# Performance work log

Measured on AMD Instinct MI355X. Metric: run time of the kernel, lower is better.

Reference implementation:

```python
import jax, jax.numpy as jnp
import numpy as np

NEG_SLOPE = 0.2
NUM_NODES = 100000
NUM_EDGES = 200000
NNZ = 1600000
IN_C = 128
OUT_C = 128
STAR = 64


def setup_inputs() -> dict:
    key = jax.random.key(0)
    ks = jax.random.split(key, 12)
    X = jax.random.normal(ks[0], (NUM_NODES, IN_C), dtype=jnp.float32)
    V = jax.random.randint(ks[1], (NNZ,), 0, NUM_NODES)
    E = jax.random.randint(ks[2], (NNZ,), 0, NUM_EDGES)
    S_features = jax.random.normal(ks[3], (NUM_EDGES, STAR), dtype=jnp.float32)
    s = 1.0 / np.sqrt(IN_C)
    Wx = jax.random.uniform(ks[4], (IN_C, OUT_C), minval=-s, maxval=s)
    bx = jax.random.uniform(ks[5], (OUT_C,), minval=-s, maxval=s)
    Wv = jax.random.uniform(ks[6], (IN_C, OUT_C), minval=-s, maxval=s)
    bv = jax.random.uniform(ks[7], (OUT_C,), minval=-s, maxval=s)
    sa = 1.0 / np.sqrt(OUT_C)
    a_vec = jax.random.uniform(ks[8], (OUT_C,), minval=-sa, maxval=sa)
    st = 1.0 / np.sqrt(OUT_C + STAR)
    Wt = jax.random.uniform(ks[9], (OUT_C + STAR, OUT_C), minval=-st, maxval=st)
    bt = jax.random.uniform(ks[10], (OUT_C,), minval=-st, maxval=st)
    return {"X": X, "V": V, "E": E, "S_features": S_features,
            "Wx": Wx, "bx": bx, "Wv": Wv, "bv": bv,
            "a_vec": a_vec, "Wt": Wt, "bt": bt}


def _segment_softmax(s, seg, num_segments):
    m = jax.ops.segment_max(s, seg, num_segments=num_segments)
    e = jnp.exp(s - m[seg])
    denom = jax.ops.segment_sum(e, seg, num_segments=num_segments)
    return e / denom[seg]


def reference(X, V, E, S_features, Wx, bx, Wv, bv, a_vec, Wt, bt):
    # DPHGNNConv forward (eval mode: dropout = identity)
    X_init = X @ Wx + bx                      # [N, out]
    X_feat = X @ Wv + bv                      # [N, out]
    scores = X_feat @ a_vec                   # [N]
    s = jax.nn.leaky_relu(scores[V], NEG_SLOPE)  # [nnz]
    w = _segment_softmax(s, E, NUM_EDGES)     # [nnz]
    Xev = X_feat[V] * w[:, None]              # [nnz, out]
    Y_v2e = jax.ops.segment_sum(Xev, E, num_segments=NUM_EDGES)
    Y_v2e = jax.nn.elu(Y_v2e)
    e_msg = jnp.concatenate([Y_v2e, S_features], axis=1)  # [E, out+star]
    Y = e_msg @ Wt + bt                       # [E, out]
    Yev = Y[E]                                # [nnz, out]
    num = jax.ops.segment_sum(Yev, V, num_segments=NUM_NODES)
    cnt = jax.ops.segment_sum(jnp.ones((NNZ,), jnp.float32), V, num_segments=NUM_NODES)
    Xn = num / jnp.maximum(cnt, 1.0)[:, None]  # scatter_mean
    Xn = jax.nn.elu(Xn)                        # is_last=False
    return Xn + X_init
```

## Files before the change

kernel.cpp:

```cpp
#include <hip/hip_runtime.h>
#include <math.h>

#define N_NODES 100000
#define N_EDGES 200000
#define NNZ_    1600000
#define INC  128
#define OUTC 128
#define STAR_ 64
#define NEG 0.2f
#define NBIN_E 391
#define NBIN_V 196
#define NBIN (NBIN_E + NBIN_V)
#define CHUNK 4000
#define NBLK_A (NNZ_/CHUNK)
#define NBLK_CVT 224
#define CAP_E 5120
#define CAP_V 9216
#define PAIR_SZ (NBIN_E*CAP_E + NBIN_V*CAP_V)
#define CAPI 288
#define CAPN 288

typedef __attribute__((ext_vector_type(8))) short bf16x8_t;
typedef __attribute__((ext_vector_type(8))) unsigned short u16x8;
typedef __attribute__((ext_vector_type(4))) float f32x4_t;

__device__ __forceinline__ float leaky(float x){ return x > 0.f ? x : NEG*x; }
__device__ __forceinline__ float elu1(float x){ return x > 0.f ? x : __expf(x)-1.f; }
__device__ __forceinline__ unsigned short f2bf(float f){
  unsigned u = __float_as_uint(f);
  unsigned r = u + 0x7FFFu + ((u >> 16) & 1u);
  return (unsigned short)(r >> 16);
}
__device__ __forceinline__ float bf2f(unsigned short h){
  return __uint_as_float(((unsigned)h) << 16);
}
__device__ __forceinline__ int padBaseD(int bin){
  return bin < NBIN_E ? bin*CAP_E : NBIN_E*CAP_E + (bin-NBIN_E)*CAP_V;
}

__global__ __launch_bounds__(256) void k_cvtA(
    const float* __restrict__ Wx, const float* __restrict__ Wv,
    const float* __restrict__ Wt,
    unsigned short* __restrict__ WcatT, unsigned short* __restrict__ WtT,
    const int* __restrict__ V, const int* __restrict__ E,
    int* __restrict__ binCur, int2* __restrict__ pair,
    int* __restrict__ vIdxE, int* __restrict__ eIdxV){
  __shared__ int hA[NBIN];
  __shared__ int baseA[NBIN];
  const int tid = threadIdx.x;

  if (blockIdx.x < NBLK_A) {
    for (int p = tid; p < NBIN; p += 256) hA[p] = 0;
    __syncthreads();
    const int start = blockIdx.x*CHUNK, end = start + CHUNK;
    for (int i = start + tid; i < end; i += 256){
      atomicAdd(&hA[E[i] >> 9], 1);
      atomicAdd(&hA[NBIN_E + (V[i] >> 9)], 1);
    }
    __syncthreads();
    for (int p = tid; p < NBIN; p += 256)
      baseA[p] = hA[p] ? padBaseD(p) + atomicAdd(&binCur[p], hA[p]) : 0;
    __syncthreads();
    for (int p = tid; p < NBIN; p += 256) hA[p] = 0;
    __syncthreads();
    for (int i = start + tid; i < end; i += 256){
      const int e = E[i], v = V[i];
      const int be = e >> 9, bv_ = NBIN_E + (v >> 9);
      const int se = baseA[be]  + atomicAdd(&hA[be],  1);
      const int sv = baseA[bv_] + atomicAdd(&hA[bv_], 1);
      pair[se] = make_int2(e, v);
      pair[sv] = make_int2(v, e);
    }
    return;
  }

  const int i = (blockIdx.x - NBLK_A)*256 + tid;
  if (i < 256*128){
    const int n = i >> 7, k = i & 127;
    const float v = (n < 128) ? Wx[k*128 + n] : Wv[k*128 + (n-128)];
    WcatT[n*128 + k] = f2bf(v);
  }
  const int j = i - 256*128;
  if (j >= 0 && j < 128*192){
    const int n = j / 192, k = j - n*192;
    WtT[n*192 + k] = f2bf(Wt[k*128 + n]);
  }
  if (blockIdx.x == NBLK_A && tid < 16){
    vIdxE[NNZ_ + tid] = 0; eIdxV[NNZ_ + tid] = 0;
  }
}

__global__ __launch_bounds__(256) void k_front2(
    const float* __restrict__ X, const unsigned short* __restrict__ WcatT,
    const float* __restrict__ bx, const float* __restrict__ bv,
    const float* __restrict__ av,
    float* __restrict__ Xinit, unsigned short* __restrict__ Xfb,
    float* __restrict__ scoresExp,
    const int2* __restrict__ pair, const int* __restrict__ binCur,
    int* __restrict__ vIdxE, int* __restrict__ cntE, int* __restrict__ startsE,
    int* __restrict__ eIdxV, int* __restrict__ cntV, int* __restrict__ startsV){
  __shared__ __align__(16) char smem[6144];
  const int tid = threadIdx.x;

  if (blockIdx.x < NBIN) {
    int* h   = (int*)smem;
    int* sc0 = h + 512;
    int* sc1 = sc0 + 512;
    const int bin = blockIdx.x;
    const bool isE = bin < NBIN_E;
    const int nb = isE ? bin : bin - NBIN_E;
    const int bucket0 = nb << 9;
    const int nBuckTot = isE ? N_EDGES : N_NODES;
    const int pstart = padBaseD(bin);
    const int n = binCur[bin];
    {
      int part = 0;
      for (int p = tid; p < bin; p += 256) part += binCur[p];
      sc0[tid] = part;
      __syncthreads();
      for (int o = 128; o; o >>= 1){ if (tid < o) sc0[tid] += sc0[tid+o]; __syncthreads(); }
    }
    const int itemBase = isE ? sc0[0] : sc0[0] - NNZ_;
    __syncthreads();
    for (int p = tid; p < 512; p += 256) h[p] = 0;
    __syncthreads();
    for (int j = tid; j < n; j += 256) atomicAdd(&h[pair[pstart + j].x & 511], 1);
    __syncthreads();
    for (int p = tid; p < 512; p += 256) sc0[p] = h[p];
    __syncthreads();
    int* a = sc0; int* b = sc1;
    for (int o = 1; o < 512; o <<= 1){
      for (int p = tid; p < 512; p += 256) b[p] = a[p] + (p >= o ? a[p-o] : 0);
      __syncthreads();
      int* t = a; a = b; b = t;
    }
    for (int p = tid; p < 512; p += 256){
      const int excl = a[p] - h[p];
      b[p] = itemBase + excl;
      const int bucket = bucket0 + p;
      if (bucket < nBuckTot){
        if (isE){ cntE[bucket] = h[p]; startsE[bucket] = itemBase + excl; }
        else    { cntV[bucket] = h[p]; startsV[bucket] = itemBase + excl; }
      }
    }
    __syncthreads();
    for (int j = tid; j < n; j += 256){
      const int2 kv = pair[pstart + j];
      const int slot = atomicAdd(&b[kv.x & 511], 1);
      if (isE) vIdxE[slot] = kv.y; else eIdxV[slot] = kv.y;
    }
    return;
  }

  unsigned short (*xb)[136] = (unsigned short (*)[136])smem;
  float* sc = (float*)(smem + 4352);
  const int lane = tid & 63, w = tid >> 6;
  const int quad = lane >> 4, l16 = lane & 15;
  const int r0 = (blockIdx.x - NBIN) * 16;
  if (tid < 16) sc[tid] = 0.f;
  {
    const int r = tid >> 4;
    const int c0 = (tid & 15) * 8;
    const float4 a4 = *(const float4*)&X[(size_t)(r0+r)*INC + c0];
    const float4 b4 = *(const float4*)&X[(size_t)(r0+r)*INC + c0 + 4];
    bf16x8_t pk;
    pk[0]=(short)f2bf(a4.x); pk[1]=(short)f2bf(a4.y); pk[2]=(short)f2bf(a4.z); pk[3]=(short)f2bf(a4.w);
    pk[4]=(short)f2bf(b4.x); pk[5]=(short)f2bf(b4.y); pk[6]=(short)f2bf(b4.z); pk[7]=(short)f2bf(b4.w);
    *(bf16x8_t*)&xb[r][c0] = pk;
  }
  __syncthreads();
  f32x4_t acc[4] = {{0,0,0,0},{0,0,0,0},{0,0,0,0},{0,0,0,0}};
  const int n_base = w*64 + l16;
  for (int s = 0; s < 4; ++s){
    const bf16x8_t af = *(const bf16x8_t*)&xb[l16][s*32 + quad*8];
    #pragma unroll
    for (int nt = 0; nt < 4; ++nt){
      const int n = n_base + nt*16;
      const bf16x8_t bf = *(const bf16x8_t*)&WcatT[(size_t)n*128 + s*32 + quad*8];
      acc[nt] = __builtin_amdgcn_mfma_f32_16x16x32_bf16(af, bf, acc[nt], 0, 0, 0);
    }
  }
  float pr[4] = {0.f, 0.f, 0.f, 0.f};
  #pragma unroll
  for (int nt = 0; nt < 4; ++nt){
    const int n = n_base + nt*16;
    const float bias = (n < 128) ? bx[n] : bv[n-128];
    #pragma unroll
    for (int r = 0; r < 4; ++r){
      const int m = quad*4 + r;
      const float val = acc[nt][r] + bias;
      if (n < 128) Xinit[(size_t)(r0+m)*OUTC + n] = val;
      else {
        Xfb[(size_t)(r0+m)*OUTC + (n-128)] = f2bf(val);
        pr[r] += val * av[n-128];
      }
    }
  }
  if (w >= 2){
    #pragma unroll
    for (int r = 0; r < 4; ++r) atomicAdd(&sc[quad*4 + r], pr[r]);
  }
  __syncthreads();
  if (tid < 16) scoresExp[r0 + tid] = __expf(leaky(sc[tid]));
}

__global__ __launch_bounds__(256) void k_edge(
    const int* __restrict__ cntE, const int* __restrict__ startsE,
    const int* __restrict__ vIdxE, const float* __restrict__ scoresExp,
    const unsigned short* __restrict__ Xfb,
    const float* __restrict__ S, const unsigned short* __restrict__ WtT,
    const float* __restrict__ bt, unsigned short* __restrict__ Ybf) {
  __shared__ int inc[CAPI + 8];
  __shared__ unsigned short msg[16][200];
  const int tid = threadIdx.x;
  const int lane = tid & 63, w = tid >> 6;
  const int e0 = blockIdx.x * 16;
  const int g16 = tid >> 4, s16 = tid & 15;

  const int st0 = startsE[e0];
  const int lim = startsE[e0 + 15] + cntE[e0 + 15] - st0;

  for (int i = tid; i < CAPI + 8; i += 256)
    inc[i] = (i < lim) ? vIdxE[st0 + i] : 0;

  {
    const float4 s4 = *(const float4*)&S[(size_t)(e0+g16)*STAR_ + s16*4];
    ushort4 pk; pk.x=f2bf(s4.x); pk.y=f2bf(s4.y); pk.z=f2bf(s4.z); pk.w=f2bf(s4.w);
    *(ushort4*)&msg[g16][128 + s16*4] = pk;
  }
  __syncthreads();

  const int e = e0 + g16;
  const int deg = cntE[e];
  const int lo  = startsE[e] - st0;
  const int c8 = s16 * 8;
  float ac[8] = {0.f,0.f,0.f,0.f,0.f,0.f,0.f,0.f};
  float wsum = 0.f;
  if (lo + deg <= CAPI) {
    for (int j = 0; j < deg; j += 8) {
      int pp[8];
      #pragma unroll
      for (int k = 0; k < 8; ++k) pp[k] = inc[lo + j + k];
      float ww[8];
      #pragma unroll
      for (int k = 0; k < 8; ++k) ww[k] = scoresExp[pp[k]];
      u16x8 xx[8];
      #pragma unroll
      for (int k = 0; k < 8; ++k)
        xx[k] = *(const u16x8*)&Xfb[(size_t)pp[k]*OUTC + c8];
      #pragma unroll
      for (int k = 0; k < 8; ++k) {
        const float wgt = (j + k < deg) ? ww[k] : 0.f;
        wsum += wgt;
        #pragma unroll
        for (int q = 0; q < 8; ++q) ac[q] += wgt * bf2f(xx[k][q]);
      }
    }
  } else {
    const int st = st0 + lo;
    for (int j = 0; j < deg; j += 8) {
      int pp[8];
      #pragma unroll
      for (int k = 0; k < 8; ++k) pp[k] = vIdxE[st + j + k];
      float ww[8];
      #pragma unroll
      for (int k = 0; k < 8; ++k) ww[k] = scoresExp[pp[k]];
      u16x8 xx[8];
      #pragma unroll
      for (int k = 0; k < 8; ++k)
        xx[k] = *(const u16x8*)&Xfb[(size_t)pp[k]*OUTC + c8];
      #pragma unroll
      for (int k = 0; k < 8; ++k) {
        const float wgt = (j + k < deg) ? ww[k] : 0.f;
        wsum += wgt;
        #pragma unroll
        for (int q = 0; q < 8; ++q) ac[q] += wgt * bf2f(xx[k][q]);
      }
    }
  }
  {
    const float invd = wsum > 0.f ? 1.f/wsum : 0.f;
    u16x8 pk;
    #pragma unroll
    for (int q = 0; q < 8; ++q) pk[q] = f2bf(elu1(ac[q]*invd));
    *(u16x8*)&msg[g16][c8] = pk;
  }
  __syncthreads();

  const int quad = lane >> 4, l16 = lane & 15;
  f32x4_t acc0 = {0,0,0,0}, acc1 = {0,0,0,0};
  const int n0 = w * 32;
  for (int s = 0; s < 6; ++s) {
    const bf16x8_t af = *(const bf16x8_t*)&msg[l16][s*32 + quad*8];
    const bf16x8_t b0 = *(const bf16x8_t*)&WtT[(size_t)(n0 + l16)*192      + s*32 + quad*8];
    const bf16x8_t b1 = *(const bf16x8_t*)&WtT[(size_t)(n0 + 16 + l16)*192 + s*32 + quad*8];
    acc0 = __builtin_amdgcn_mfma_f32_16x16x32_bf16(af, b0, acc0, 0, 0, 0);
    acc1 = __builtin_amdgcn_mfma_f32_16x16x32_bf16(af, b1, acc1, 0, 0, 0);
  }
  const float bt0 = bt[n0 + l16], bt1 = bt[n0 + 16 + l16];
  #pragma unroll
  for (int r = 0; r < 4; ++r) {
    const int m = quad*4 + r;
    Ybf[(size_t)(e0+m)*OUTC + n0 + l16]      = f2bf(acc0[r] + bt0);
    Ybf[(size_t)(e0+m)*OUTC + n0 + 16 + l16] = f2bf(acc1[r] + bt1);
  }
}

__global__ __launch_bounds__(256) void k_node(
    const int* __restrict__ cntV, const int* __restrict__ startsV,
    const int* __restrict__ eIdxV,
    const unsigned short* __restrict__ Ybf, float* __restrict__ out) {
  __shared__ int elds[CAPN + 8];
  const int tid = threadIdx.x;
  const int sub = tid & 31, grp = tid >> 5;
  const int v0 = blockIdx.x * 8;

  const int st0 = startsV[v0];
  const int lim = startsV[v0 + 7] + cntV[v0 + 7] - st0;
  for (int i = tid; i < CAPN + 8; i += 256)
    elds[i] = (i < lim) ? eIdxV[st0 + i] : 0;
  __syncthreads();

  const int v = v0 + grp;
  const int c4 = sub * 4;
  const int deg = cntV[v];
  const int lo  = startsV[v] - st0;
  float a0=0.f, a1=0.f, a2=0.f, a3=0.f;
  if (lo + deg <= CAPN) {
    for (int j = 0; j < deg; j += 8) {
      int ee[8];
      #pragma unroll
      for (int k = 0; k < 8; ++k) ee[k] = elds[lo + j + k];
      ushort4 yy[8];
      #pragma unroll
      for (int k = 0; k < 8; ++k)
        yy[k] = *(const ushort4*)&Ybf[(size_t)ee[k]*OUTC + c4];
      #pragma unroll
      for (int k = 0; k < 8; ++k) {
        const float pz = (j + k < deg) ? 1.f : 0.f;
        a0 += pz * bf2f(yy[k].x); a1 += pz * bf2f(yy[k].y);
        a2 += pz * bf2f(yy[k].z); a3 += pz * bf2f(yy[k].w);
      }
    }
  } else {
    const int st = st0 + lo;
    for (int j = 0; j < deg; j += 8) {
      int ee[8];
      #pragma unroll
      for (int k = 0; k < 8; ++k) ee[k] = eIdxV[st + j + k];
      ushort4 yy[8];
      #pragma unroll
      for (int k = 0; k < 8; ++k)
        yy[k] = *(const ushort4*)&Ybf[(size_t)ee[k]*OUTC + c4];
      #pragma unroll
      for (int k = 0; k < 8; ++k) {
        const float pz = (j + k < deg) ? 1.f : 0.f;
        a0 += pz * bf2f(yy[k].x); a1 += pz * bf2f(yy[k].y);
        a2 += pz * bf2f(yy[k].z); a3 += pz * bf2f(yy[k].w);
      }
    }
  }
  const float invd = 1.f / fmaxf((float)deg, 1.f);
  float4 o = *(float4*)&out[(size_t)v*OUTC + c4];
  o.x = elu1(a0*invd) + o.x;
  o.y = elu1(a1*invd) + o.y;
  o.z = elu1(a2*invd) + o.z;
  o.w = elu1(a3*invd) + o.w;
  *(float4*)&out[(size_t)v*OUTC + c4] = o;
}

extern "C" void kernel_launch(void* const* d_in, const int* in_sizes, int n_in,
                              void* d_out, int out_size, void* d_ws, size_t ws_size,
                              hipStream_t stream) {
  const float* X  = (const float*)d_in[0];
  const int*   V  = (const int*)d_in[1];
  const int*   E  = (const int*)d_in[2];
  const float* S  = (const float*)d_in[3];
  const float* Wx = (const float*)d_in[4];
  const float* bx = (const float*)d_in[5];
  const float* Wv = (const float*)d_in[6];
  const float* bv = (const float*)d_in[7];
  const float* av = (const float*)d_in[8];
  const float* Wt = (const float*)d_in[9];
  const float* bt = (const float*)d_in[10];
  float* out = (float*)d_out;

  char* ws = (char*)d_ws;
  size_t off = 0;
  auto alloc = [&](size_t bytes) -> void* {
    off = (off + 255) & ~(size_t)255;
    void* p = ws + off; off += bytes; return p;
  };
  unsigned short* Xfb   = (unsigned short*)alloc((size_t)N_NODES*OUTC*2);
  unsigned short* Ybf   = (unsigned short*)alloc((size_t)N_EDGES*OUTC*2);
  float* scoresExp = (float*)alloc((size_t)N_NODES*4);
  unsigned short* WcatT = (unsigned short*)alloc((size_t)256*128*2);
  unsigned short* WtT   = (unsigned short*)alloc((size_t)128*192*2);
  int2* pair   = (int2*)alloc((size_t)PAIR_SZ*8);
  int* binCur  = (int*)alloc((size_t)NBIN*4);
  int* cntE    = (int*)alloc((size_t)N_EDGES*4);
  int* cntV    = (int*)alloc((size_t)N_NODES*4);
  int* startsE = (int*)alloc((size_t)N_EDGES*4);
  int* startsV = (int*)alloc((size_t)N_NODES*4);
  int* vIdxE   = (int*)alloc((size_t)(NNZ_+16)*4);
  int* eIdxV   = (int*)alloc((size_t)(NNZ_+16)*4);

  hipMemsetAsync(binCur, 0, (size_t)NBIN*4, stream);
  k_cvtA<<<NBLK_A + NBLK_CVT, 256, 0, stream>>>(Wx, Wv, Wt, WcatT, WtT,
                                                V, E, binCur, pair, vIdxE, eIdxV);
  k_front2<<<NBIN + N_NODES/16, 256, 0, stream>>>(X, WcatT, bx, bv, av, out, Xfb, scoresExp,
                                                  pair, binCur,
                                                  vIdxE, cntE, startsE,
                                                  eIdxV, cntV, startsV);
  k_edge<<<N_EDGES/16, 256, 0, stream>>>(cntE, startsE, vIdxE, scoresExp,
                                         Xfb, S, WtT, bt, Ybf);
  k_node<<<N_NODES/8, 256, 0, stream>>>(cntV, startsV, eIdxV, Ybf, out);
}
```

Before: 473.3 us.

## Regroup kernels: co-schedule binning pass A with projection GEMM, split pass B

Weight conversion moves into a small standalone kernel that also seeds binCur with each bin's padded base, so the memset is dropped. Pass A of the binning (the first histogram and scatter) now shares a launch with the X projection GEMM instead of with weight conversion. Pass B runs as its own kernel with 512 threads per block. The aim is to overlap the scatter-heavy binning with the GEMM and to simplify the scans, at the cost of an extra launch and a dependency ordering that now puts the GEMM before pass B.

Result: faster. 462.5 us (-2.3%).

```diff
diff --git a/kernel.cpp b/kernel.cpp
--- a/kernel.cpp
+++ b/kernel.cpp
@@ -13,7 +13,6 @@
 #define NBIN (NBIN_E + NBIN_V)
 #define CHUNK 4000
 #define NBLK_A (NNZ_/CHUNK)
-#define NBLK_CVT 224
 #define CAP_E 5120
 #define CAP_V 9216
 #define PAIR_SZ (NBIN_E*CAP_E + NBIN_V*CAP_V)
@@ -38,15 +37,40 @@
   return bin < NBIN_E ? bin*CAP_E : NBIN_E*CAP_E + (bin-NBIN_E)*CAP_V;
 }
 
-__global__ __launch_bounds__(256) void k_cvtA(
-    const float* __restrict__ Wx, const float* __restrict__ Wv,
-    const float* __restrict__ Wt,
-    unsigned short* __restrict__ WcatT, unsigned short* __restrict__ WtT,
+__global__ void k_cvt(const float* __restrict__ Wx, const float* __restrict__ Wv,
+                      const float* __restrict__ Wt,
+                      unsigned short* __restrict__ WcatT, unsigned short* __restrict__ WtT,
+                      int* __restrict__ binCur,
+                      int* __restrict__ vIdxE, int* __restrict__ eIdxV){
+  const int i = blockIdx.x*256 + threadIdx.x;
+  if (i < 256*128){
+    const int n = i >> 7, k = i & 127;
+    const float v = (n < 128) ? Wx[k*128 + n] : Wv[k*128 + (n-128)];
+    WcatT[n*128 + k] = f2bf(v);
+  }
+  const int j = i - 256*128;
+  if (j >= 0 && j < 128*192){
+    const int n = j / 192, k = j - n*192;
+    WtT[n*192 + k] = f2bf(Wt[k*128 + n]);
+  }
+  if (blockIdx.x == 0){
+    for (int p = threadIdx.x; p < NBIN; p += 256) binCur[p] = padBaseD(p);
+    if (threadIdx.x < 16){ vIdxE[NNZ_ + threadIdx.x] = 0; eIdxV[NNZ_ + threadIdx.x] = 0; }
+  }
+}
+
+__global__ __launch_bounds__(256) void k_front(
+    const float* __restrict__ X, const unsigned short* __restrict__ WcatT,
+    const float* __restrict__ bx, const float* __restrict__ bv,
+    const float* __restrict__ av,
+    float* __restrict__ Xinit, unsigned short* __restrict__ Xfb,
+    float* __restrict__ scoresExp,
     const int* __restrict__ V, const int* __restrict__ E,
-    int* __restrict__ binCur, int2* __restrict__ pair,
-    int* __restrict__ vIdxE, int* __restrict__ eIdxV){
+    int* __restrict__ binCur, int2* __restrict__ pair){
   __shared__ int hA[NBIN];
   __shared__ int baseA[NBIN];
+  __shared__ unsigned short xb[16][136];
+  __shared__ float sc[16];
   const int tid = threadIdx.x;
 
   if (blockIdx.x < NBLK_A) {
@@ -59,7 +83,7 @@
     }
     __syncthreads();
     for (int p = tid; p < NBIN; p += 256)
-      baseA[p] = hA[p] ? padBaseD(p) + atomicAdd(&binCur[p], hA[p]) : 0;
+      baseA[p] = hA[p] ? atomicAdd(&binCur[p], hA[p]) : 0;
     __syncthreads();
     for (int p = tid; p < NBIN; p += 256) hA[p] = 0;
     __syncthreads();
@@ -74,89 +98,9 @@
     return;
   }
 
-  const int i = (blockIdx.x - NBLK_A)*256 + tid;
-  if (i < 256*128){
-    const int n = i >> 7, k = i & 127;
-    const float v = (n < 128) ? Wx[k*128 + n] : Wv[k*128 + (n-128)];
-    WcatT[n*128 + k] = f2bf(v);
-  }
-  const int j = i - 256*128;
-  if (j >= 0 && j < 128*192){
-    const int n = j / 192, k = j - n*192;
-    WtT[n*192 + k] = f2bf(Wt[k*128 + n]);
-  }
-  if (blockIdx.x == NBLK_A && tid < 16){
-    vIdxE[NNZ_ + tid] = 0; eIdxV[NNZ_ + tid] = 0;
-  }
-}
-
-__global__ __launch_bounds__(256) void k_front2(
-    const float* __restrict__ X, const unsigned short* __restrict__ WcatT,
-    const float* __restrict__ bx, const float* __restrict__ bv,
-    const float* __restrict__ av,
-    float* __restrict__ Xinit, unsigned short* __restrict__ Xfb,
-    float* __restrict__ scoresExp,
-    const int2* __restrict__ pair, const int* __restrict__ binCur,
-    int* __restrict__ vIdxE, int* __restrict__ cntE, int* __restrict__ startsE,
-    int* __restrict__ eIdxV, int* __restrict__ cntV, int* __restrict__ startsV){
-  __shared__ __align__(16) char smem[6144];
-  const int tid = threadIdx.x;
-
-  if (blockIdx.x < NBIN) {
-    int* h   = (int*)smem;
-    int* sc0 = h + 512;
-    int* sc1 = sc0 + 512;
-    const int bin = blockIdx.x;
-    const bool isE = bin < NBIN_E;
-    const int nb = isE ? bin : bin - NBIN_E;
-    const int bucket0 = nb << 9;
-    const int nBuckTot = isE ? N_EDGES : N_NODES;
-    const int pstart = padBaseD(bin);
-    const int n = binCur[bin];
-    {
-      int part = 0;
-      for (int p = tid; p < bin; p += 256) part += binCur[p];
-      sc0[tid] = part;
-      __syncthreads();
-      for (int o = 128; o; o >>= 1){ if (tid < o) sc0[tid] += sc0[tid+o]; __syncthreads(); }
-    }
-    const int itemBase = isE ? sc0[0] : sc0[0] - NNZ_;
-    __syncthreads();
-    for (int p = tid; p < 512; p += 256) h[p] = 0;
-    __syncthreads();
-    for (int j = tid; j < n; j += 256) atomicAdd(&h[pair[pstart + j].x & 511], 1);
-    __syncthreads();
-    for (int p = tid; p < 512; p += 256) sc0[p] = h[p];
-    __syncthreads();
-    int* a = sc0; int* b = sc1;
-    for (int o = 1; o < 512; o <<= 1){
-      for (int p = tid; p < 512; p += 256) b[p] = a[p] + (p >= o ? a[p-o] : 0);
-      __syncthreads();
-      int* t = a; a = b; b = t;
-    }
-    for (int p = tid; p < 512; p += 256){
-      const int excl = a[p] - h[p];
-      b[p] = itemBase + excl;
-      const int bucket = bucket0 + p;
-      if (bucket < nBuckTot){
-        if (isE){ cntE[bucket] = h[p]; startsE[bucket] = itemBase + excl; }
-        else    { cntV[bucket] = h[p]; startsV[bucket] = itemBase + excl; }
-      }
-    }
-    __syncthreads();
-    for (int j = tid; j < n; j += 256){
-      const int2 kv = pair[pstart + j];
-      const int slot = atomicAdd(&b[kv.x & 511], 1);
-      if (isE) vIdxE[slot] = kv.y; else eIdxV[slot] = kv.y;
-    }
-    return;
-  }
-
-  unsigned short (*xb)[136] = (unsigned short (*)[136])smem;
-  float* sc = (float*)(smem + 4352);
   const int lane = tid & 63, w = tid >> 6;
   const int quad = lane >> 4, l16 = lane & 15;
-  const int r0 = (blockIdx.x - NBIN) * 16;
+  const int r0 = (blockIdx.x - NBLK_A) * 16;
   if (tid < 16) sc[tid] = 0.f;
   {
     const int r = tid >> 4;
@@ -202,6 +146,57 @@
   }
   __syncthreads();
   if (tid < 16) scoresExp[r0 + tid] = __expf(leaky(sc[tid]));
+}
+
+__global__ __launch_bounds__(512) void k_binB(const int2* __restrict__ pair,
+    const int* __restrict__ binCur,
+    int* __restrict__ vIdxE, int* __restrict__ cntE, int* __restrict__ startsE,
+    int* __restrict__ eIdxV, int* __restrict__ cntV, int* __restrict__ startsV){
+  __shared__ int h[512], sc0[512], sc1[512];
+  const int bin = blockIdx.x;
+  const bool isE = bin < NBIN_E;
+  const int nb = isE ? bin : bin - NBIN_E;
+  const int bucket0 = nb << 9;
+  const int nBuckTot = isE ? N_EDGES : N_NODES;
+  const int pstart = padBaseD(bin);
+  const int n = binCur[bin] - pstart;
+  const int tid = threadIdx.x;
+  {
+    int part = 0;
+    for (int p = tid; p < bin; p += 512) part += binCur[p] - padBaseD(p);
+    sc0[tid] = part;
+    __syncthreads();
+    for (int o = 256; o; o >>= 1){ if (tid < o) sc0[tid] += sc0[tid+o]; __syncthreads(); }
+  }
+  const int itemBase = sc0[0] - (isE ? 0 : NNZ_);
+  __syncthreads();
+  h[tid] = 0;
+  __syncthreads();
+  for (int j = tid; j < n; j += 512) atomicAdd(&h[pair[pstart + j].x & 511], 1);
+  __syncthreads();
+  sc0[tid] = h[tid];
+  __syncthreads();
+  int* a = sc0; int* b = sc1;
+  for (int o = 1; o < 512; o <<= 1){
+    b[tid] = a[tid] + (tid >= o ? a[tid-o] : 0);
+    __syncthreads();
+    int* t = a; a = b; b = t;
+  }
+  {
+    const int excl = a[tid] - h[tid];
+    b[tid] = itemBase + excl;
+    const int bucket = bucket0 + tid;
+    if (bucket < nBuckTot){
+      if (isE){ cntE[bucket] = h[tid]; startsE[bucket] = itemBase + excl; }
+      else    { cntV[bucket] = h[tid]; startsV[bucket] = itemBase + excl; }
+    }
+  }
+  __syncthreads();
+  for (int j = tid; j < n; j += 512){
+    const int2 kv = pair[pstart + j];
+    const int slot = atomicAdd(&b[kv.x & 511], 1);
+    if (isE) vIdxE[slot] = kv.y; else eIdxV[slot] = kv.y;
+  }
 }
 
 __global__ __launch_bounds__(256) void k_edge(
@@ -405,13 +400,13 @@
   int* vIdxE   = (int*)alloc((size_t)(NNZ_+16)*4);
   int* eIdxV   = (int*)alloc((size_t)(NNZ_+16)*4);
 
-  hipMemsetAsync(binCur, 0, (size_t)NBIN*4, stream);
-  k_cvtA<<<NBLK_A + NBLK_CVT, 256, 0, stream>>>(Wx, Wv, Wt, WcatT, WtT,
-                                                V, E, binCur, pair, vIdxE, eIdxV);
-  k_front2<<<NBIN + N_NODES/16, 256, 0, stream>>>(X, WcatT, bx, bv, av, out, Xfb, scoresExp,
-                                                  pair, binCur,
-                                                  vIdxE, cntE, startsE,
-                                                  eIdxV, cntV, startsV);
+  k_cvt<<<(256*128 + 128*192 + 255)/256, 256, 0, stream>>>(Wx, Wv, Wt, WcatT, WtT,
+                                                           binCur, vIdxE, eIdxV);
+  k_front<<<NBLK_A + N_NODES/16, 256, 0, stream>>>(X, WcatT, bx, bv, av, out, Xfb, scoresExp,
+                                                   V, E, binCur, pair);
+  k_binB<<<NBIN, 512, 0, stream>>>(pair, binCur,
+                                   vIdxE, cntE, startsE,
+                                   eIdxV, cntV, startsV);
   k_edge<<<N_EDGES/16, 256, 0, stream>>>(cntE, startsE, vIdxE, scoresExp,
                                          Xfb, S, WtT, bt, Ybf);
   k_node<<<N_NODES/8, 256, 0, stream>>>(cntV, startsV, eIdxV, Ybf, out);
```
